# Optimization experiments

Hardware: AMD Instinct MI355X
Metric: run time of the kernel (lower is better)

## Reference

```python
import jax, jax.numpy as jnp
import numpy as np

B, S, H = 2, 2048, 2048
N_HEADS = 16
HEAD_DIM = H // N_HEADS  # 128


def apply_rotary(x, cos, sin):
    # x: (B, n_heads, S, head_dim); cos/sin: (S, head_dim//2)
    d = x.shape[-1] // 2
    x1, x2 = x[..., :d], x[..., d:]
    c = cos[None, None, :x.shape[2]]
    s = sin[None, None, :x.shape[2]]
    return jnp.concatenate([x1 * c - x2 * s, x2 * c + x1 * s], axis=-1)


def setup_inputs() -> dict:
    key = jax.random.key(0)
    k1, k2, k3 = jax.random.split(key, 3)
    x = jax.random.normal(k1, (B, S, H), dtype=jnp.float32)
    qkv_w = jax.random.normal(k2, (3 * H, H), dtype=jnp.float32) * (1.0 / np.sqrt(H))
    o_w = jax.random.normal(k3, (H, H), dtype=jnp.float32) * (1.0 / np.sqrt(H))
    # rotary tables, half head_dim
    inv_freq = 1.0 / (10000.0 ** (jnp.arange(0, HEAD_DIM // 2, dtype=jnp.float32) / (HEAD_DIM // 2)))
    t = jnp.arange(S, dtype=jnp.float32)
    freqs = jnp.outer(t, inv_freq)  # (S, head_dim//2)
    cos, sin = jnp.cos(freqs), jnp.sin(freqs)
    # True = masked (strictly upper triangular)
    causal_mask = jnp.triu(jnp.ones((S, S), dtype=bool), k=1)
    return {"x": x, "qkv_w": qkv_w, "o_w": o_w, "cos": cos, "sin": sin,
            "causal_mask": causal_mask}


def reference(x, qkv_w, o_w, cos, sin, causal_mask):
    Bx, Sx, Hx = x.shape
    qkv = jnp.einsum('bsh,oh->bso', x, qkv_w)  # (B,S,3H)
    qkv = qkv.reshape(Bx, Sx, 3, N_HEADS, HEAD_DIM)
    q, k, v = qkv[:, :, 0], qkv[:, :, 1], qkv[:, :, 2]
    q = jnp.transpose(q, (0, 2, 1, 3))  # (B,nh,S,hd)
    k = jnp.transpose(k, (0, 2, 1, 3))
    v = jnp.transpose(v, (0, 2, 1, 3))
    q = apply_rotary(q, cos, sin)
    k = apply_rotary(k, cos, sin)
    scale = 1.0 / jnp.sqrt(jnp.asarray(HEAD_DIM, dtype=x.dtype))
    attn = jnp.einsum('bnqd,bnkd->bnqk', q, k) * scale
    attn = jnp.where(causal_mask[None, None], -jnp.inf, attn)
    attn = jax.nn.softmax(attn, axis=-1)
    out = jnp.einsum('bnqk,bnkd->bnqd', attn, v)
    out = jnp.transpose(out, (0, 2, 1, 3)).reshape(Bx, Sx, Hx)
    return jnp.einsum('bsh,oh->bso', out, o_w)
```

## Files before the change

### kernel.cpp

```cpp
#include <hip/hip_runtime.h>
#include <hip/hip_bf16.h>
#include <stdint.h>

typedef __attribute__((ext_vector_type(4))) float f32x4;
typedef __attribute__((ext_vector_type(8))) short s16x8;
typedef __attribute__((ext_vector_type(4))) short s16x4;

#define SWZ(g, row) ((((g) & ~7) | (((g) ^ ((row) & 7)) & 7)))

__device__ __forceinline__ unsigned short f2bf(float f) {
  unsigned u = __builtin_bit_cast(unsigned, f);
  u += 0x7fffu + ((u >> 16) & 1u);
  return (unsigned short)(u >> 16);
}

__device__ __forceinline__ void gld16(const void* g, void* l) {
  __builtin_amdgcn_global_load_lds(
      (const __attribute__((address_space(1))) void*)g,
      (__attribute__((address_space(3))) void*)l, 16, 0, 0);
}

__global__ void cvt_f32_to_bf16(const float* __restrict__ src,
                                unsigned short* __restrict__ dst, int n4) {
  int i = blockIdx.x * blockDim.x + threadIdx.x;
  if (i >= n4) return;
  float4 v = ((const float4*)src)[i];
  s16x4 o;
  o[0] = (short)f2bf(v.x); o[1] = (short)f2bf(v.y);
  o[2] = (short)f2bf(v.z); o[3] = (short)f2bf(v.w);
  ((s16x4*)dst)[i] = o;
}

#define STAGE384(BB, KT) \
  { char* dA = smem + (BB) * 65536; \
    char* dB = dA + 16384; \
    _Pragma("unroll") for (int rr = 0; rr < 2; ++rr) { \
      const int G = rr * 512 + tid; const int row = G >> 3, g = G & 7; \
      gld16((const char*)(Aorg + (size_t)row * 2048 + (size_t)(KT) * 64) + (SWZ(g, row) << 4), \
            dA + rr * 8192 + tid * 16); } \
    _Pragma("unroll") for (int rr = 0; rr < 6; ++rr) { \
      const int G = rr * 512 + tid; const int row = G >> 3, g = G & 7; \
      gld16((const char*)(Borg + (size_t)row * 2048 + (size_t)(KT) * 64) + (SWZ(g, row) << 4), \
            dB + rr * 8192 + tid * 16); } }

#define RD384(AV, BV, KS) \
  _Pragma("unroll") for (int j = 0; j < 4; ++j) { \
    const int ra = wm * 64 + j * 16 + lg; \
    AV[j] = *(const s16x8*)(sA + ra * 128 + (SWZ(4 * (KS) + hg, ra) << 4)); } \
  _Pragma("unroll") for (int b = 0; b < 6; ++b) { \
    const int cb = (b >> 1) * 128 + wn * 16 + (b & 1) * 64 + lg; \
    BV[b] = *(const s16x8*)(sB + cb * 128 + (SWZ(4 * (KS) + hg, cb) << 4)); }

#define MM384(AV, BV) \
  _Pragma("unroll") for (int j = 0; j < 4; ++j) \
    _Pragma("unroll") for (int b = 0; b < 6; ++b) \
      acc[j][b] = __builtin_amdgcn_mfma_f32_16x16x32_bf16(AV[j], BV[b], acc[j][b], 0, 0, 0);

__global__ __launch_bounds__(512, 1) void gemm_qkv_384(
    const unsigned short* __restrict__ A,
    const unsigned short* __restrict__ Bt,
    const float* __restrict__ cosT, const float* __restrict__ sinT,
    unsigned short* __restrict__ qOut, unsigned short* __restrict__ kOut,
    unsigned short* __restrict__ vtOut)
{
  __shared__ char smem[131072];
  const int tid = (int)threadIdx.x;
  const int wid = tid >> 6, l = tid & 63;
  const int lg = l & 15, hg = l >> 4;
  const int wm = wid >> 2, wn = wid & 3;
  const int s = ((int)blockIdx.x & 7) * 64 + ((int)blockIdx.x >> 3);
  const int bm0 = (s & 31) * 128, bn0 = (s >> 5) * 384;

  const unsigned short* Aorg = A + (size_t)bm0 * 2048;
  const unsigned short* Borg = Bt + (size_t)bn0 * 2048;

  f32x4 acc[4][6] = {};

  STAGE384(0, 0)
  for (int t = 0; t < 31; ++t) {
    STAGE384((t & 1) ^ 1, t + 1)
    asm volatile("s_waitcnt vmcnt(8)" ::: "memory");
    __builtin_amdgcn_s_barrier();
    const char* sA = smem + (t & 1) * 65536;
    const char* sB = sA + 16384;
    const int ksA = wm, ksB = 1 - wm;
    s16x8 avA[4], bvA[6], avB[4], bvB[6];
    RD384(avA, bvA, ksA)
    RD384(avB, bvB, ksB)
    __builtin_amdgcn_s_setprio(1);
    MM384(avA, bvA)
    __builtin_amdgcn_s_setprio(0);
    asm volatile("s_waitcnt lgkmcnt(0)" ::: "memory");
    __builtin_amdgcn_s_barrier();
    __builtin_amdgcn_sched_barrier(0);
    __builtin_amdgcn_s_setprio(1);
    MM384(avB, bvB)
    __builtin_amdgcn_s_setprio(0);
  }
  {
    asm volatile("s_waitcnt vmcnt(0)" ::: "memory");
    __builtin_amdgcn_s_barrier();
    const char* sA = smem + 65536;
    const char* sB = sA + 16384;
    s16x8 avA[4], bvA[6], avB[4], bvB[6];
    RD384(avA, bvA, 0)
    RD384(avB, bvB, 1)
    MM384(avA, bvA)
    MM384(avB, bvB)
  }

  #pragma unroll
  for (int j = 0; j < 4; ++j) {
    const int grow0 = bm0 + wm * 64 + j * 16 + hg * 4;
    const int b_ = grow0 >> 11;
    #pragma unroll
    for (int cg = 0; cg < 3; ++cg) {
      const int og = (bn0 >> 7) + cg;
      const int tt = og >> 4, h = og & 15;
      const int d = wn * 16 + lg;
      if (tt < 2) {
        unsigned short* dst = (tt == 0) ? qOut : kOut;
        #pragma unroll
        for (int r = 0; r < 4; ++r) {
          const int gr = grow0 + r;
          const int s1 = gr & 2047;
          const float x1 = acc[j][cg * 2 + 0][r];
          const float x2 = acc[j][cg * 2 + 1][r];
          const float cv = cosT[s1 * 64 + d];
          const float sv = sinT[s1 * 64 + d];
          const size_t base = (((size_t)b_ * 16 + h) * 2048 + s1) * 128;
          dst[base + d]      = f2bf(x1 * cv - x2 * sv);
          dst[base + d + 64] = f2bf(x2 * cv + x1 * sv);
        }
      } else {
        const int s0 = grow0 & 2047;
        s16x4 p1, p2;
        #pragma unroll
        for (int r = 0; r < 4; ++r) {
          p1[r] = (short)f2bf(acc[j][cg * 2 + 0][r]);
          p2[r] = (short)f2bf(acc[j][cg * 2 + 1][r]);
        }
        *(s16x4*)(vtOut + (((size_t)b_ * 16 + h) * 128 + d)      * 2048 + s0) = p1;
        *(s16x4*)(vtOut + (((size_t)b_ * 16 + h) * 128 + d + 64) * 2048 + s0) = p2;
      }
    }
  }
}

#define STAGEOP(BB, KT) \
  { char* dA = smem + (BB) * 49152; \
    char* dB = dA + 16384; \
    _Pragma("unroll") for (int rr = 0; rr < 2; ++rr) { \
      const int G = rr * 512 + tid; const int row = G >> 3, g = G & 7; \
      gld16((const char*)(Aorg + (size_t)row * 2048 + (size_t)(KT) * 64) + (SWZ(g, row) << 4), \
            dA + rr * 8192 + tid * 16); } \
    _Pragma("unroll") for (int rr = 0; rr < 4; ++rr) { \
      const int G = rr * 512 + tid; const int row = G >> 3, g = G & 7; \
      gld16((const char*)(Borg + (size_t)row * 2048 + (size_t)(KT) * 64) + (SWZ(g, row) << 4), \
            dB + rr * 8192 + tid * 16); } }

#define RDOP(AV, BV, KS) \
  _Pragma("unroll") for (int j = 0; j < 4; ++j) { \
    const int ra = wm * 64 + j * 16 + lg; \
    AV[j] = *(const s16x8*)(sA + ra * 128 + (SWZ(4 * (KS) + hg, ra) << 4)); } \
  _Pragma("unroll") for (int b = 0; b < 4; ++b) { \
    const int cb = b * 64 + wn * 16 + lg; \
    BV[b] = *(const s16x8*)(sB + cb * 128 + (SWZ(4 * (KS) + hg, cb) << 4)); }

#define MMOP(AV, BV) \
  _Pragma("unroll") for (int j = 0; j < 4; ++j) \
    _Pragma("unroll") for (int b = 0; b < 4; ++b) \
      acc[j][b] = __builtin_amdgcn_mfma_f32_16x16x32_bf16(AV[j], BV[b], acc[j][b], 0, 0, 0);

__global__ __launch_bounds__(512, 1) void gemm_op_256(
    const unsigned short* __restrict__ A,
    const unsigned short* __restrict__ Bt,
    float* __restrict__ C)
{
  __shared__ char smem[98304];
  const int tid = (int)threadIdx.x;
  const int wid = tid >> 6, l = tid & 63;
  const int lg = l & 15, hg = l >> 4;
  const int wm = wid >> 2, wn = wid & 3;
  const int s = ((int)blockIdx.x & 7) * 32 + ((int)blockIdx.x >> 3);
  const int bm0 = (s & 31) * 128, bn0 = (s >> 5) * 256;

  const unsigned short* Aorg = A + (size_t)bm0 * 2048;
  const unsigned short* Borg = Bt + (size_t)bn0 * 2048;

  f32x4 acc[4][4] = {};

  STAGEOP(0, 0)
  for (int t = 0; t < 31; ++t) {
    STAGEOP((t & 1) ^ 1, t + 1)
    asm volatile("s_waitcnt vmcnt(6)" ::: "memory");
    __builtin_amdgcn_s_barrier();
    const char* sA = smem + (t & 1) * 49152;
    const char* sB = sA + 16384;
    const int ksA = wm, ksB = 1 - wm;
    s16x8 avA[4], bvA[4], avB[4], bvB[4];
    RDOP(avA, bvA, ksA)
    RDOP(avB, bvB, ksB)
    __builtin_amdgcn_s_setprio(1);
    MMOP(avA, bvA)
    __builtin_amdgcn_s_setprio(0);
    asm volatile("s_waitcnt lgkmcnt(0)" ::: "memory");
    __builtin_amdgcn_s_barrier();
    __builtin_amdgcn_sched_barrier(0);
    __builtin_amdgcn_s_setprio(1);
    MMOP(avB, bvB)
    __builtin_amdgcn_s_setprio(0);
  }
  {
    asm volatile("s_waitcnt vmcnt(0)" ::: "memory");
    __builtin_amdgcn_s_barrier();
    const char* sA = smem + 49152;
    const char* sB = sA + 16384;
    s16x8 avA[4], bvA[4], avB[4], bvB[4];
    RDOP(avA, bvA, 0)
    RDOP(avB, bvB, 1)
    MMOP(avA, bvA)
    MMOP(avB, bvB)
  }

  #pragma unroll
  for (int j = 0; j < 4; ++j) {
    const int row0 = bm0 + wm * 64 + j * 16 + hg * 4;
    #pragma unroll
    for (int b = 0; b < 4; ++b) {
      const int col = bn0 + b * 64 + wn * 16 + lg;
      #pragma unroll
      for (int r = 0; r < 4; ++r)
        C[(size_t)(row0 + r) * 2048 + col] = acc[j][b][r];
    }
  }
}

__global__ __launch_bounds__(256) void attn_fwd(
    const unsigned short* __restrict__ Qp, const unsigned short* __restrict__ Kp,
    const unsigned short* __restrict__ Vt, unsigned short* __restrict__ AO)
{
  __shared__ char sK[16384];
  __shared__ char sV[16384];
  __shared__ char sP[8192];

  const int tid = (int)threadIdx.x, w = tid >> 6, l = tid & 63;
  const int lg = l & 15, hg = l >> 4;
  const int bid = (int)blockIdx.x;
  const int p = bid >> 8, c = bid & 255;
  const int j = c >> 5, bh = c & 31;
  const int qt = (p == 0) ? j : (p == 1) ? 31 - j : (p == 2) ? 8 + j : 23 - j;
  const size_t qkBase = (size_t)bh * 2048 * 128;
  const int qw0 = qt * 64 + w * 16;
  const int qi = qw0 + lg;

  s16x8 qf[4];
  for (int ks = 0; ks < 4; ++ks)
    qf[ks] = *(const s16x8*)(Qp + qkBase + (size_t)(qw0 + lg) * 128 + ks * 32 + hg * 8);

  f32x4 acc_o[8] = {};
  float mrun = -1e30f, lrun = 0.f;
  const float SCALE = 0.08838834764831845f;
  const float L2E = 1.4426950408889634f;
  const float CS = SCALE * L2E;

  const int nkv = qt + 1;
  for (int kv = 0; kv < nkv; ++kv) {
    const int kv0 = kv * 64;
    __syncthreads();
    for (int i = 0; i < 4; ++i) {
      const int G = w * 256 + i * 64 + l;
      const int rk = G >> 4, gk = G & 15;
      gld16((const char*)(Kp + qkBase + (size_t)(kv0 + rk) * 128) + (SWZ(gk, rk) << 4),
            sK + w * 4096 + i * 1024);
      const int rv = G >> 3, gv = G & 7;
      gld16((const char*)(Vt + qkBase + (size_t)rv * 2048 + kv0) + (SWZ(gv, rv) << 4),
            sV + w * 4096 + i * 1024);
    }
    asm volatile("s_waitcnt vmcnt(0)" ::: "memory");
    __syncthreads();

    f32x4 accs[4] = {};
    for (int ks = 0; ks < 4; ++ks)
      for (int kf = 0; kf < 4; ++kf) {
        const int row = kf * 16 + lg;
        const int g = SWZ(4 * ks + hg, row);
        s16x8 kfrag = *(const s16x8*)(sK + row * 256 + (g << 4));
        accs[kf] = __builtin_amdgcn_mfma_f32_16x16x32_bf16(kfrag, qf[ks], accs[kf], 0, 0, 0);
      }

    const bool diag = (kv == qt);
    float raw[4][4];
    float mt = -1e30f;
    #pragma unroll
    for (int kf = 0; kf < 4; ++kf)
      #pragma unroll
      for (int r = 0; r < 4; ++r) {
        float s = accs[kf][r];
        if (diag) {
          const int jj = kv0 + kf * 16 + hg * 4 + r;
          s = (jj > qi) ? -1e30f : s;
        }
        raw[kf][r] = s;
        mt = fmaxf(mt, s);
      }
    mt = fmaxf(mt, __shfl_xor(mt, 16));
    mt = fmaxf(mt, __shfl_xor(mt, 32));
    mt *= SCALE;
    if (!__all(mt - mrun <= 8.0f)) {
      const float mnew = fmaxf(mrun, mt);
      const float alpha = exp2f((mrun - mnew) * L2E);
      float ar[4];
      #pragma unroll
      for (int r = 0; r < 4; ++r) ar[r] = __shfl(alpha, hg * 4 + r);
      #pragma unroll
      for (int f = 0; f < 8; ++f)
        #pragma unroll
        for (int r = 0; r < 4; ++r) acc_o[f][r] *= ar[r];
      lrun *= alpha;
      mrun = mnew;
    }
    const float mL = mrun * L2E;
    float ls = 0.f;
    char* pw = sP + w * 2048;
    #pragma unroll
    for (int kf = 0; kf < 4; ++kf) {
      s16x4 pk;
      #pragma unroll
      for (int r = 0; r < 4; ++r) {
        const float e = exp2f(raw[kf][r] * CS - mL);
        ls += e;
        pk[r] = (short)f2bf(e);
      }
      const int j0 = kf * 16 + hg * 4;
      *(s16x4*)(pw + lg * 128 + (SWZ(j0 >> 3, lg) << 4) + ((j0 * 2) & 15)) = pk;
    }
    ls += __shfl_xor(ls, 16);
    ls += __shfl_xor(ls, 32);
    lrun += ls;
    asm volatile("" ::: "memory");

    for (int jc = 0; jc < 2; ++jc) {
      const int gp = SWZ(hg + 4 * jc, lg);
      s16x8 pa = *(const s16x8*)(pw + lg * 128 + (gp << 4));
      for (int f = 0; f < 8; ++f) {
        const int rv = f * 16 + lg;
        const int gv = SWZ(hg + 4 * jc, rv);
        s16x8 vb = *(const s16x8*)(sV + rv * 128 + (gv << 4));
        acc_o[f] = __builtin_amdgcn_mfma_f32_16x16x32_bf16(pa, vb, acc_o[f], 0, 0, 0);
      }
    }
  }

  float linv[4];
  for (int r = 0; r < 4; ++r) linv[r] = 1.0f / __shfl(lrun, hg * 4 + r);
  const int b = bh >> 4, h = bh & 15;
  for (int f = 0; f < 8; ++f) {
    const int d = h * 128 + f * 16 + lg;
    for (int r = 0; r < 4; ++r) {
      const int srow = qw0 + hg * 4 + r;
      AO[((size_t)(b * 2048 + srow)) * 2048 + d] = f2bf(acc_o[f][r] * linv[r]);
    }
  }
}

extern "C" void kernel_launch(void* const* d_in, const int* in_sizes, int n_in,
                              void* d_out, int out_size, void* d_ws, size_t ws_size,
                              hipStream_t stream) {
  const float* x    = (const float*)d_in[0];
  const float* qkvw = (const float*)d_in[1];
  const float* ow   = (const float*)d_in[2];
  const float* cosT = (const float*)d_in[3];
  const float* sinT = (const float*)d_in[4];
  float* out = (float*)d_out;

  unsigned short* X16  = (unsigned short*)d_ws;
  unsigned short* W16  = X16  + (size_t)8388608;
  unsigned short* OW16 = W16  + (size_t)12582912;
  unsigned short* Qp   = OW16 + (size_t)4194304;
  unsigned short* Kp   = Qp   + (size_t)8388608;
  unsigned short* Vtp  = Kp   + (size_t)8388608;
  unsigned short* AO   = Vtp  + (size_t)8388608;

  cvt_f32_to_bf16<<<8192, 256, 0, stream>>>(x, X16, 2097152);
  cvt_f32_to_bf16<<<12288, 256, 0, stream>>>(qkvw, W16, 3145728);
  cvt_f32_to_bf16<<<4096, 256, 0, stream>>>(ow, OW16, 1048576);

  gemm_qkv_384<<<512, 512, 0, stream>>>(X16, W16, cosT, sinT, Qp, Kp, Vtp);

  attn_fwd<<<1024, 256, 0, stream>>>(Qp, Kp, Vtp, AO);

  gemm_op_256<<<256, 512, 0, stream>>>(AO, OW16, out);
}
```

Measured before the change: 236.4 us.

## Split GEMM k-steps into four barrier-fenced phases and fuse bf16 conversions

Both GEMM main loops now run in four smaller phases. Each phase reads the A fragments once per k-substep and only a chunk of B fragments from LDS, then runs a burst of MFMAs bracketed by barriers and priority changes. The old scheme, where wave halves staggered their k-substeps, is gone. This cuts live fragment registers and interleaves LDS reads with MFMA work more finely, but adds twice as many block barriers per iteration. Separately, the three fp32-to-bf16 conversion launches are merged into one kernel to reduce launch overhead.

```diff
diff --git a/kernel.cpp b/kernel.cpp
--- a/kernel.cpp
+++ b/kernel.cpp
@@ -20,15 +20,19 @@
       (__attribute__((address_space(3))) void*)l, 16, 0, 0);
 }
 
-__global__ void cvt_f32_to_bf16(const float* __restrict__ src,
-                                unsigned short* __restrict__ dst, int n4) {
+__global__ void cvt_all(const float* __restrict__ x, const float* __restrict__ qkvw,
+                        const float* __restrict__ ow, unsigned short* __restrict__ X16,
+                        unsigned short* __restrict__ W16, unsigned short* __restrict__ OW16) {
   int i = blockIdx.x * blockDim.x + threadIdx.x;
-  if (i >= n4) return;
-  float4 v = ((const float4*)src)[i];
+  const float* src; unsigned short* dst; int off;
+  if (i < 2097152)      { src = x;    dst = X16;  off = i; }
+  else if (i < 5242880) { src = qkvw; dst = W16;  off = i - 2097152; }
+  else                  { src = ow;   dst = OW16; off = i - 5242880; }
+  float4 v = ((const float4*)src)[off];
   s16x4 o;
   o[0] = (short)f2bf(v.x); o[1] = (short)f2bf(v.y);
   o[2] = (short)f2bf(v.z); o[3] = (short)f2bf(v.w);
-  ((s16x4*)dst)[i] = o;
+  ((s16x4*)dst)[off] = o;
 }
 
 #define STAGE384(BB, KT) \
@@ -43,18 +47,32 @@
       gld16((const char*)(Borg + (size_t)row * 2048 + (size_t)(KT) * 64) + (SWZ(g, row) << 4), \
             dB + rr * 8192 + tid * 16); } }
 
-#define RD384(AV, BV, KS) \
+#define RDA(KS) \
   _Pragma("unroll") for (int j = 0; j < 4; ++j) { \
     const int ra = wm * 64 + j * 16 + lg; \
-    AV[j] = *(const s16x8*)(sA + ra * 128 + (SWZ(4 * (KS) + hg, ra) << 4)); } \
-  _Pragma("unroll") for (int b = 0; b < 6; ++b) { \
-    const int cb = (b >> 1) * 128 + wn * 16 + (b & 1) * 64 + lg; \
-    BV[b] = *(const s16x8*)(sB + cb * 128 + (SWZ(4 * (KS) + hg, cb) << 4)); }
-
-#define MM384(AV, BV) \
+    av[j] = *(const s16x8*)(sA + ra * 128 + (SWZ(4 * (KS) + hg, ra) << 4)); }
+
+#define RDB(KS, CH) \
+  _Pragma("unroll") for (int b = 0; b < 3; ++b) { \
+    const int bb = (CH) * 3 + b; \
+    const int cb = (bb >> 1) * 128 + wn * 16 + (bb & 1) * 64 + lg; \
+    bv[b] = *(const s16x8*)(sB + cb * 128 + (SWZ(4 * (KS) + hg, cb) << 4)); }
+
+#define MM12(CH) \
   _Pragma("unroll") for (int j = 0; j < 4; ++j) \
-    _Pragma("unroll") for (int b = 0; b < 6; ++b) \
-      acc[j][b] = __builtin_amdgcn_mfma_f32_16x16x32_bf16(AV[j], BV[b], acc[j][b], 0, 0, 0);
+    _Pragma("unroll") for (int b = 0; b < 3; ++b) \
+      acc[j][(CH) * 3 + b] = __builtin_amdgcn_mfma_f32_16x16x32_bf16( \
+          av[j], bv[b], acc[j][(CH) * 3 + b], 0, 0, 0);
+
+#define PH_PRE \
+  __builtin_amdgcn_s_barrier(); \
+  asm volatile("s_waitcnt lgkmcnt(0)" ::: "memory"); \
+  __builtin_amdgcn_sched_barrier(0); \
+  __builtin_amdgcn_s_setprio(1);
+
+#define PH_POST \
+  __builtin_amdgcn_s_setprio(0); \
+  __builtin_amdgcn_s_barrier();
 
 __global__ __launch_bounds__(512, 1) void gemm_qkv_384(
     const unsigned short* __restrict__ A,
@@ -83,30 +101,22 @@
     __builtin_amdgcn_s_barrier();
     const char* sA = smem + (t & 1) * 65536;
     const char* sB = sA + 16384;
-    const int ksA = wm, ksB = 1 - wm;
-    s16x8 avA[4], bvA[6], avB[4], bvB[6];
-    RD384(avA, bvA, ksA)
-    RD384(avB, bvB, ksB)
-    __builtin_amdgcn_s_setprio(1);
-    MM384(avA, bvA)
-    __builtin_amdgcn_s_setprio(0);
-    asm volatile("s_waitcnt lgkmcnt(0)" ::: "memory");
-    __builtin_amdgcn_s_barrier();
-    __builtin_amdgcn_sched_barrier(0);
-    __builtin_amdgcn_s_setprio(1);
-    MM384(avB, bvB)
-    __builtin_amdgcn_s_setprio(0);
+    s16x8 av[4], bv[3];
+    RDA(0) RDB(0, 0)  PH_PRE  MM12(0)  PH_POST
+    RDB(0, 1)         PH_PRE  MM12(1)  PH_POST
+    RDA(1) RDB(1, 1)  PH_PRE  MM12(1)  PH_POST
+    RDB(1, 0)         PH_PRE  MM12(0)  PH_POST
   }
   {
     asm volatile("s_waitcnt vmcnt(0)" ::: "memory");
     __builtin_amdgcn_s_barrier();
     const char* sA = smem + 65536;
     const char* sB = sA + 16384;
-    s16x8 avA[4], bvA[6], avB[4], bvB[6];
-    RD384(avA, bvA, 0)
-    RD384(avB, bvB, 1)
-    MM384(avA, bvA)
-    MM384(avB, bvB)
+    s16x8 av[4], bv[3];
+    RDA(0) RDB(0, 0)  PH_PRE  MM12(0)  PH_POST
+    RDB(0, 1)         PH_PRE  MM12(1)  PH_POST
+    RDA(1) RDB(1, 1)  PH_PRE  MM12(1)  PH_POST
+    RDB(1, 0)         PH_PRE  MM12(0)  PH_POST
   }
 
   #pragma unroll
@@ -159,18 +169,16 @@
       gld16((const char*)(Borg + (size_t)row * 2048 + (size_t)(KT) * 64) + (SWZ(g, row) << 4), \
             dB + rr * 8192 + tid * 16); } }
 
-#define RDOP(AV, BV, KS) \
-  _Pragma("unroll") for (int j = 0; j < 4; ++j) { \
-    const int ra = wm * 64 + j * 16 + lg; \
-    AV[j] = *(const s16x8*)(sA + ra * 128 + (SWZ(4 * (KS) + hg, ra) << 4)); } \
-  _Pragma("unroll") for (int b = 0; b < 4; ++b) { \
-    const int cb = b * 64 + wn * 16 + lg; \
-    BV[b] = *(const s16x8*)(sB + cb * 128 + (SWZ(4 * (KS) + hg, cb) << 4)); }
-
-#define MMOP(AV, BV) \
+#define RDBO(KS, CH) \
+  _Pragma("unroll") for (int b = 0; b < 2; ++b) { \
+    const int cb = ((CH) * 2 + b) * 64 + wn * 16 + lg; \
+    bv[b] = *(const s16x8*)(sB + cb * 128 + (SWZ(4 * (KS) + hg, cb) << 4)); }
+
+#define MMO(CH) \
   _Pragma("unroll") for (int j = 0; j < 4; ++j) \
-    _Pragma("unroll") for (int b = 0; b < 4; ++b) \
-      acc[j][b] = __builtin_amdgcn_mfma_f32_16x16x32_bf16(AV[j], BV[b], acc[j][b], 0, 0, 0);
+    _Pragma("unroll") for (int b = 0; b < 2; ++b) \
+      acc[j][(CH) * 2 + b] = __builtin_amdgcn_mfma_f32_16x16x32_bf16( \
+          av[j], bv[b], acc[j][(CH) * 2 + b], 0, 0, 0);
 
 __global__ __launch_bounds__(512, 1) void gemm_op_256(
     const unsigned short* __restrict__ A,
@@ -197,30 +205,22 @@
     __builtin_amdgcn_s_barrier();
     const char* sA = smem + (t & 1) * 49152;
     const char* sB = sA + 16384;
-    const int ksA = wm, ksB = 1 - wm;
-    s16x8 avA[4], bvA[4], avB[4], bvB[4];
-    RDOP(avA, bvA, ksA)
-    RDOP(avB, bvB, ksB)
-    __builtin_amdgcn_s_setprio(1);
-    MMOP(avA, bvA)
-    __builtin_amdgcn_s_setprio(0);
-    asm volatile("s_waitcnt lgkmcnt(0)" ::: "memory");
-    __builtin_amdgcn_s_barrier();
-    __builtin_amdgcn_sched_barrier(0);
-    __builtin_amdgcn_s_setprio(1);
-    MMOP(avB, bvB)
-    __builtin_amdgcn_s_setprio(0);
+    s16x8 av[4], bv[2];
+    RDA(0) RDBO(0, 0)  PH_PRE  MMO(0)  PH_POST
+    RDBO(0, 1)         PH_PRE  MMO(1)  PH_POST
+    RDA(1) RDBO(1, 1)  PH_PRE  MMO(1)  PH_POST
+    RDBO(1, 0)         PH_PRE  MMO(0)  PH_POST
   }
   {
     asm volatile("s_waitcnt vmcnt(0)" ::: "memory");
     __builtin_amdgcn_s_barrier();
     const char* sA = smem + 49152;
     const char* sB = sA + 16384;
-    s16x8 avA[4], bvA[4], avB[4], bvB[4];
-    RDOP(avA, bvA, 0)
-    RDOP(avB, bvB, 1)
-    MMOP(avA, bvA)
-    MMOP(avB, bvB)
+    s16x8 av[4], bv[2];
+    RDA(0) RDBO(0, 0)  PH_PRE  MMO(0)  PH_POST
+    RDBO(0, 1)         PH_PRE  MMO(1)  PH_POST
+    RDA(1) RDBO(1, 1)  PH_PRE  MMO(1)  PH_POST
+    RDBO(1, 0)         PH_PRE  MMO(0)  PH_POST
   }
 
   #pragma unroll
@@ -382,9 +382,7 @@
   unsigned short* Vtp  = Kp   + (size_t)8388608;
   unsigned short* AO   = Vtp  + (size_t)8388608;
 
-  cvt_f32_to_bf16<<<8192, 256, 0, stream>>>(x, X16, 2097152);
-  cvt_f32_to_bf16<<<12288, 256, 0, stream>>>(qkvw, W16, 3145728);
-  cvt_f32_to_bf16<<<4096, 256, 0, stream>>>(ow, OW16, 1048576);
+  cvt_all<<<24576, 256, 0, stream>>>(x, qkvw, ow, X16, W16, OW16);
 
   gemm_qkv_384<<<512, 512, 0, stream>>>(X16, W16, cosT, sinT, Qp, Kp, Vtp);
 
```

New measurement: 253.0 us. 1.07x slower.
